# Kernel optimization log

Measured on AMD Instinct MI355X. Metric: run time of the kernel, lower is better.

The kernel has to match this reference:

```python
import jax, jax.numpy as jnp
import numpy as np

G, N, E, F, D = 4096, 64, 256, 64, 128
H1, H2 = 16, 2
EP = 32768
EPS = 1e-15
MAX_LOGSTD = 10.0


def setup_inputs() -> dict:
    key = jax.random.key(0)
    ks = jax.random.split(key, 16)
    def lin(k, i, o):
        return (jax.random.normal(k, (i, o), jnp.float32) / np.sqrt(i)).astype(jnp.float32)
    inp = {}
    inp["x"] = jax.random.normal(ks[0], (G, N, F), jnp.float32)
    inp["edge_index"] = jax.random.randint(ks[1], (G, 2, E), 0, N, dtype=jnp.int32)
    inp["edge_weight"] = jax.random.uniform(ks[2], (G, E), jnp.float32)
    inp["pos_edges"] = jax.random.randint(ks[3], (2, EP), 0, G, dtype=jnp.int32)
    inp["neg_edges"] = jax.random.randint(ks[4], (2, EP), 0, G, dtype=jnp.int32)
    inp["eps"] = jax.random.normal(ks[5], (G, D), jnp.float32)
    inp["W_gcn1"] = lin(ks[6], F, D); inp["b_gcn1"] = jnp.zeros((D,), jnp.float32)
    inp["W_fc1"] = lin(ks[7], D, H1); inp["b_fc1"] = jnp.zeros((H1,), jnp.float32)
    inp["W_fc2"] = lin(ks[8], H1, H2); inp["b_fc2"] = jnp.zeros((H2,), jnp.float32)
    inp["W_c1"] = lin(ks[9], D, 2 * D); inp["b_c1"] = jnp.zeros((2 * D,), jnp.float32)
    inp["W_mu"] = lin(ks[10], 2 * D, D); inp["b_mu"] = jnp.zeros((D,), jnp.float32)
    inp["W_ls"] = lin(ks[11], 2 * D, D); inp["b_ls"] = jnp.zeros((D,), jnp.float32)
    inp["emb"] = jax.random.normal(ks[12], (G, D), jnp.float32)
    inp["W_lin1"] = lin(ks[13], 2 * D, 2 * D); inp["b_lin1"] = jnp.zeros((2 * D,), jnp.float32)
    inp["W_lin2"] = lin(ks[14], 2 * D, 2 * D); inp["b_lin2"] = jnp.zeros((2 * D,), jnp.float32)
    return inp


def gcn_conv(x, src, dst, w, W, b, n):
    # PyG GCNConv: add self-loops (weight 1), sym-normalize, aggregate at target (col).
    xw = x @ W                                      # [n, out]
    deg = jnp.zeros((n,), xw.dtype).at[dst].add(w) + 1.0
    dinv = jax.lax.rsqrt(deg)
    norm = dinv[src] * w * dinv[dst]
    agg = jnp.zeros_like(xw).at[dst].add(xw[src] * norm[:, None])
    agg = agg + xw * (dinv * dinv)[:, None]         # self-loop term
    return agg + b


def sage_graph(x, ei, w, W_gcn1, b_gcn1, W_fc1, b_fc1, W_fc2, b_fc2):
    src, dst = ei[0], ei[1]
    h = gcn_conv(x, src, dst, w, W_gcn1, b_gcn1, N)          # [N, D]
    a1 = jnp.tanh(h @ W_fc1 + b_fc1)                         # [N, H1]
    S = jax.nn.softmax(a1 @ W_fc2 + b_fc2, axis=1)           # [N, 2]
    # get_laplacian(normalization='sym'): L = I - D^{-1/2} A D^{-1/2}, deg from row
    deg = jnp.zeros((N,), x.dtype).at[src].add(w)
    dinv = jnp.where(deg > 0, jax.lax.rsqrt(jnp.maximum(deg, 1e-30)), 0.0)
    lw = -dinv[src] * w * dinv[dst]
    L = jnp.zeros((N, N), x.dtype).at[src, dst].add(lw) + jnp.eye(N, dtype=x.dtype)
    new_adj = S.T @ (L @ S)                                  # [2, 2]
    norm_adj = new_adj / jnp.maximum(jnp.sum(jnp.abs(new_adj), axis=1, keepdims=True), 1e-12)
    diag = jnp.diagonal(norm_adj)
    pos_penalty = jnp.mean((diag - 1.0) ** 2)                # MSE vs ones(2)
    g_emb = jnp.mean(S.T @ h, axis=0)                        # [D]
    return g_emb, pos_penalty


def gcn_conv_unw(x, src, dst, W, b, n):
    return gcn_conv(x, src, dst, jnp.ones(src.shape, x.dtype), W, b, n)


def reference(x, edge_index, edge_weight, pos_edges, neg_edges, eps,
              W_gcn1, b_gcn1, W_fc1, b_fc1, W_fc2, b_fc2,
              W_c1, b_c1, W_mu, b_mu, W_ls, b_ls, emb,
              W_lin1, b_lin1, W_lin2, b_lin2):
    g_embs, pens = jax.vmap(sage_graph,
                            in_axes=(0, 0, 0, None, None, None, None, None, None))(
        x, edge_index, edge_weight, W_gcn1, b_gcn1, W_fc1, b_fc1, W_fc2, b_fc2)
    positive_penalty = jnp.mean(pens)
    # VGAE encode over graph-level graph (dropout in eval mode = identity)
    ps, pd = pos_edges[0], pos_edges[1]
    h = jax.nn.relu(gcn_conv_unw(g_embs, ps, pd, W_c1, b_c1, G))
    mu = gcn_conv_unw(h, ps, pd, W_mu, b_mu, G)
    logstd = jnp.minimum(gcn_conv_unw(h, ps, pd, W_ls, b_ls, G), MAX_LOGSTD)
    z = mu + eps * jnp.exp(logstd)                            # reparametrize
    zc = jnp.concatenate([emb, z], axis=-1)                   # [G, 2D]
    def pred(ei):
        fx = zc[ei[0]] @ W_lin1 + b_lin1
        fy = zc[ei[1]] @ W_lin2 + b_lin2
        return jax.nn.sigmoid(jnp.sum(fx * fy, axis=1))
    pos_pred = pred(pos_edges)
    neg_pred = pred(neg_edges)
    rec_loss = -jnp.mean(jnp.log(pos_pred + EPS)) - jnp.mean(jnp.log(1.0 - neg_pred + EPS))
    kl = -0.5 * jnp.mean(jnp.sum(1.0 + 2.0 * logstd - mu ** 2 - jnp.exp(2.0 * logstd), axis=1))
    pre_loss = rec_loss + kl / G
    return pre_loss, positive_penalty, pos_pred, neg_pred
```

## Files before the change

kernel.cpp:

```cpp
#include <hip/hip_runtime.h>
#include <hip/hip_bf16.h>
#include <math.h>

#define GG   4096
#define NNODE 64
#define EEDGE 256
#define FFEAT 64
#define DDIM 128
#define EP   32768

__global__ void k_prep(const float* __restrict__ Wg, const float* __restrict__ Wf1,
                       const float* __restrict__ bf1, const float* __restrict__ bg,
                       float* __restrict__ Wgf1, float* __restrict__ bcomb,
                       float* __restrict__ bg32, int* __restrict__ icnt_g) {
    int t = threadIdx.x;
    for (int o = t; o < 1024; o += 256) {
        int r = o >> 4, j = o & 15;
        int kk = r >> 2, q = r & 3;
        int f = q * 16 + kk;
        float s = 0.f;
        for (int d = 0; d < 128; ++d) s += Wg[f * 128 + d] * Wf1[d * 16 + j];
        Wgf1[o] = s;
    }
    if (t < 16) {
        float s = bf1[t];
        for (int d = 0; d < 128; ++d) s += bg[d] * Wf1[d * 16 + t];
        bcomb[t] = s;
    }
    if (t >= 128) bg32[t - 128] = 32.0f * bg[t - 128];
    for (int i = t; i < 4096; i += 256) icnt_g[i] = 0;
}

__global__ __launch_bounds__(256) void k_pg(
    const float* __restrict__ x, const int* __restrict__ ei, const float* __restrict__ ew,
    const float* __restrict__ Wgf1, const float* __restrict__ bcomb,
    const float* __restrict__ Wf2, const float* __restrict__ bf2,
    float* __restrict__ Qh, float* __restrict__ pens)
{
    __shared__ __align__(16) float sm[6656];
    float* xs    = sm;
    float* Wp    = sm + 4352;
    int*   lsrc  = (int*)(sm + 5376);
    float* lnrm  = sm + 5632;
    int*   icnt  = (int*)(sm + 5888);
    int*   offs  = (int*)(sm + 5952);
    int*   curs  = (int*)(sm + 6016);
    float* degw  = sm + 6080;
    float* dinvs = sm + 6144;
    float* deg2s = sm + 6208;
    float* dinv2s= sm + 6272;
    float* Ss    = sm + 6336;
    float* LSs   = sm + 6464;
    float* bcs   = sm + 6592;
    float* Wf2s  = sm + 6608;
    float* bf2s  = sm + 6640;

    const int g = blockIdx.x;
    const int t = threadIdx.x;
    const float* xg = x + (size_t)g * 4096;

    int es, ed; float wv;
    {
        const int* eg = ei + (size_t)g * 512;
        es = eg[t];
        ed = eg[256 + t];
        wv = ew[(size_t)g * 256 + t];
        for (int i = t; i < 1024; i += 256) {
            int n = i >> 4, k = (i & 15) * 4;
            *(float4*)&xs[n * 68 + k] = *(const float4*)&xg[n * 64 + k];
        }
        *(float4*)&Wp[t * 4] = *(const float4*)&Wgf1[t * 4];
        if (t < 16) bcs[t] = bcomb[t];
        if (t < 32) Wf2s[t] = Wf2[t];
        if (t < 2)  bf2s[t] = bf2[t];
        if (t < 64) { icnt[t] = 0; degw[t] = 1.0f; deg2s[t] = 0.0f; }
        if (t < 128) LSs[t] = 0.0f;
    }
    __syncthreads();

    atomicAdd(&icnt[ed], 1);
    atomicAdd(&degw[ed], wv);
    atomicAdd(&deg2s[es], wv);
    __syncthreads();

    if (t < 64) {
        int v = icnt[t], own = v;
        for (int o = 1; o < 64; o <<= 1) { int u = __shfl_up(v, o); if (t >= o) v += u; }
        int excl = v - own;
        offs[t] = excl; curs[t] = excl;
        dinvs[t] = rsqrtf(degw[t]);
        float dg = deg2s[t];
        dinv2s[t] = dg > 0.0f ? rsqrtf(fmaxf(dg, 1e-30f)) : 0.0f;
    }
    __syncthreads();

    float lw;
    {
        int pos = atomicAdd(&curs[ed], 1);
        lsrc[pos] = es;
        lnrm[pos] = dinvs[es] * wv * dinvs[ed];
        lw = -dinv2s[es] * wv * dinv2s[ed];
    }
    __syncthreads();

    const int n = t >> 2, q = t & 3, base = q * 16;
    float Av[16];
    {
        float sc = dinvs[n] * dinvs[n];
        const float* xrow = &xs[n * 68 + base];
        *(float4*)&Av[0]  = *(const float4*)&xrow[0];
        *(float4*)&Av[4]  = *(const float4*)&xrow[4];
        *(float4*)&Av[8]  = *(const float4*)&xrow[8];
        *(float4*)&Av[12] = *(const float4*)&xrow[12];
#pragma unroll
        for (int kk = 0; kk < 16; ++kk) Av[kk] *= sc;
        int o = offs[n], c = icnt[n];
        for (int j = 0; j < c; ++j) {
            int s = lsrc[o + j];
            float nm = lnrm[o + j];
            const float* xr = &xs[s * 68 + base];
            float4 X0 = *(const float4*)&xr[0];
            float4 X1 = *(const float4*)&xr[4];
            float4 X2 = *(const float4*)&xr[8];
            float4 X3 = *(const float4*)&xr[12];
            Av[0]  += X0.x * nm; Av[1]  += X0.y * nm; Av[2]  += X0.z * nm; Av[3]  += X0.w * nm;
            Av[4]  += X1.x * nm; Av[5]  += X1.y * nm; Av[6]  += X1.z * nm; Av[7]  += X1.w * nm;
            Av[8]  += X2.x * nm; Av[9]  += X2.y * nm; Av[10] += X2.z * nm; Av[11] += X2.w * nm;
            Av[12] += X3.x * nm; Av[13] += X3.y * nm; Av[14] += X3.z * nm; Av[15] += X3.w * nm;
        }
        __syncthreads();
        float* xw = &xs[n * 68 + base];
        *(float4*)&xw[0]  = *(float4*)&Av[0];
        *(float4*)&xw[4]  = *(float4*)&Av[4];
        *(float4*)&xw[8]  = *(float4*)&Av[8];
        *(float4*)&xw[12] = *(float4*)&Av[12];
    }
    __syncthreads();

    {
        float pj[16];
#pragma unroll
        for (int j = 0; j < 16; ++j) pj[j] = 0.f;
#pragma unroll
        for (int kk = 0; kk < 16; ++kk) {
            float a = Av[kk];
            const float* wr = &Wp[((kk << 2) + q) << 4];
            float4 w0 = *(const float4*)&wr[0];
            float4 w1 = *(const float4*)&wr[4];
            float4 w2 = *(const float4*)&wr[8];
            float4 w3 = *(const float4*)&wr[12];
            pj[0]  += a * w0.x; pj[1]  += a * w0.y; pj[2]  += a * w0.z; pj[3]  += a * w0.w;
            pj[4]  += a * w1.x; pj[5]  += a * w1.y; pj[6]  += a * w1.z; pj[7]  += a * w1.w;
            pj[8]  += a * w2.x; pj[9]  += a * w2.y; pj[10] += a * w2.z; pj[11] += a * w2.w;
            pj[12] += a * w3.x; pj[13] += a * w3.y; pj[14] += a * w3.z; pj[15] += a * w3.w;
        }
#pragma unroll
        for (int j = 0; j < 16; ++j) {
            pj[j] += __shfl_xor(pj[j], 1);
            pj[j] += __shfl_xor(pj[j], 2);
        }
        float z0 = bf2s[0], z1 = bf2s[1];
#pragma unroll
        for (int j = 0; j < 16; ++j) {
            float aj = tanhf(pj[j] + bcs[j]);
            z0 += aj * Wf2s[2 * j];
            z1 += aj * Wf2s[2 * j + 1];
        }
        float m = fmaxf(z0, z1);
        float e0 = expf(z0 - m), e1 = expf(z1 - m);
        float inv = 1.0f / (e0 + e1);
        if (q == 0) { Ss[n * 2] = e0 * inv; Ss[n * 2 + 1] = e1 * inv; }
    }
    __syncthreads();

    {
        float s0 = Ss[ed * 2], s1 = Ss[ed * 2 + 1];
        atomicAdd(&LSs[es * 2],     lw * s0);
        atomicAdd(&LSs[es * 2 + 1], lw * s1);
    }
    __syncthreads();

    if (t < 64) {
        float s0 = Ss[t * 2], s1 = Ss[t * 2 + 1];
        float l0 = s0 + LSs[t * 2], l1 = s1 + LSs[t * 2 + 1];
        float p00 = s0 * l0, p01 = s0 * l1, p10 = s1 * l0, p11 = s1 * l1;
        for (int o = 32; o; o >>= 1) {
            p00 += __shfl_down(p00, o); p01 += __shfl_down(p01, o);
            p10 += __shfl_down(p10, o); p11 += __shfl_down(p11, o);
        }
        if (t == 0) {
            float r0 = fmaxf(fabsf(p00) + fabsf(p01), 1e-12f);
            float r1 = fmaxf(fabsf(p10) + fabsf(p11), 1e-12f);
            float d0 = p00 / r0 - 1.0f, d1 = p11 / r1 - 1.0f;
            pens[g] = 0.5f * (d0 * d0 + d1 * d1);
        }
    }
    {
        int k = t & 63, p = t >> 6;
        float qk = 0.f;
#pragma unroll 4
        for (int nn = 0; nn < 16; ++nn)
            qk += xs[(p * 16 + nn) * 68 + k];
        Wp[p * 64 + k] = qk;
    }
    __syncthreads();
    if (t < 64)
        Qh[(size_t)g * 64 + t] = 0.5f * (Wp[t] + Wp[64 + t] + Wp[128 + t] + Wp[192 + t]);
}

__global__ void k_cnt(const int* __restrict__ pd, int* __restrict__ icnt) {
    int e = blockIdx.x * 256 + threadIdx.x;
    atomicAdd(&icnt[pd[e]], 1);
}

__global__ void k_scan(const int* __restrict__ icnt, int* __restrict__ offs,
                       int* __restrict__ curs, float* __restrict__ dinv) {
    __shared__ int wsum[4];
    int t = threadIdx.x;
    int base = t * 16;
    int l0,l1,l2,l3,l4,l5,l6,l7,l8,l9,l10,l11,l12,l13,l14,l15;
    l0=icnt[base+0]; l1=icnt[base+1]; l2=icnt[base+2]; l3=icnt[base+3];
    l4=icnt[base+4]; l5=icnt[base+5]; l6=icnt[base+6]; l7=icnt[base+7];
    l8=icnt[base+8]; l9=icnt[base+9]; l10=icnt[base+10]; l11=icnt[base+11];
    l12=icnt[base+12]; l13=icnt[base+13]; l14=icnt[base+14]; l15=icnt[base+15];
    int s = l0+l1+l2+l3+l4+l5+l6+l7+l8+l9+l10+l11+l12+l13+l14+l15;
    int lane = t & 63, w = t >> 6;
    int v = s;
    for (int o = 1; o < 64; o <<= 1) { int u = __shfl_up(v, o); if (lane >= o) v += u; }
    if (lane == 63) wsum[w] = v;
    __syncthreads();
    int woff = 0;
    for (int i = 0; i < 4; ++i) if (i < w) woff += wsum[i];
    int run = woff + v - s;
#define SC(L, I) offs[base+(I)] = run; curs[base+(I)] = run; \
    dinv[base+(I)] = rsqrtf((float)(L) + 1.0f); run += L;
    SC(l0,0) SC(l1,1) SC(l2,2) SC(l3,3) SC(l4,4) SC(l5,5) SC(l6,6) SC(l7,7)
    SC(l8,8) SC(l9,9) SC(l10,10) SC(l11,11) SC(l12,12) SC(l13,13) SC(l14,14) SC(l15,15)
#undef SC
}

__global__ void k_place(const int* __restrict__ pe, const float* __restrict__ dinv,
                        int* __restrict__ curs, int* __restrict__ csr_src,
                        float* __restrict__ csr_nrm) {
    int e = blockIdx.x * 256 + threadIdx.x;
    int s = pe[e], d = pe[EP + e];
    int pos = atomicAdd(&curs[d], 1);
    csr_src[pos] = s;
    csr_nrm[pos] = dinv[s] * dinv[d];
}

__global__ void k_gather128(const int* __restrict__ offs, const int* __restrict__ icnt,
                            const int* __restrict__ csr_src, const float* __restrict__ csr_nrm,
                            const float* __restrict__ dinv, const float* __restrict__ in,
                            float* __restrict__ out) {
    int g = blockIdx.x, d = threadIdx.x;
    float dv = dinv[g];
    float acc = in[(size_t)g * 128 + d] * dv * dv;
    int o = offs[g], c = icnt[g];
    for (int j = 0; j < c; ++j)
        acc += in[(size_t)csr_src[o + j] * 128 + d] * csr_nrm[o + j];
    out[(size_t)g * 128 + d] = acc;
}

__global__ void k_gather256(const int* __restrict__ offs, const int* __restrict__ icnt,
                            const int* __restrict__ csr_src, const float* __restrict__ csr_nrm,
                            const float* __restrict__ dinv, const float* __restrict__ in,
                            float* __restrict__ out) {
    int g = blockIdx.x, d = threadIdx.x;
    float dv = dinv[g];
    float acc = in[(size_t)g * 256 + d] * dv * dv;
    int o = offs[g], c = icnt[g];
    for (int j = 0; j < c; ++j)
        acc += in[(size_t)csr_src[o + j] * 256 + d] * csr_nrm[o + j];
    out[(size_t)g * 256 + d] = acc;
}

__global__ __launch_bounds__(256) void k_gemm(
    const float* __restrict__ A,
    const float* __restrict__ B0, const float* __restrict__ bias0, float* __restrict__ C0,
    const float* __restrict__ B1, const float* __restrict__ bias1, float* __restrict__ C1,
    int M, int K, int N, int dorelu)
{
    __shared__ __align__(16) float lds[2 * 4352];
    const float* B = B0; const float* bias = bias0; float* C = C0;
    int by = blockIdx.y;
    if (B1 != nullptr && by >= (int)(gridDim.y >> 1)) {
        B = B1; bias = bias1; C = C1; by -= (gridDim.y >> 1);
    }
    const int mb = blockIdx.x * 64, nbb = by * 64;
    const int t = threadIdx.x;
    const int tm4 = (t >> 4) * 4, tn4 = (t & 15) * 4;
    const int ma = t >> 2, ka = (t & 3) * 8;
    const int kb = t >> 3, nb8 = (t & 7) * 8;

    float4 pa0, pa1, pb0, pb1;
#define LOADT(K0) { \
    const float* Ap = &A[(size_t)(mb + ma) * K + (K0) + ka]; \
    pa0 = *(const float4*)Ap; pa1 = *(const float4*)(Ap + 4); \
    const float* Bp = &B[(size_t)((K0) + kb) * N + nbb + nb8]; \
    pb0 = *(const float4*)Bp; pb1 = *(const float4*)(Bp + 4); }
#define STORET(BUF) { \
    float* At_ = lds + (BUF) * 4352; \
    At_[(ka + 0) * 68 + ma] = pa0.x; At_[(ka + 1) * 68 + ma] = pa0.y; \
    At_[(ka + 2) * 68 + ma] = pa0.z; At_[(ka + 3) * 68 + ma] = pa0.w; \
    At_[(ka + 4) * 68 + ma] = pa1.x; At_[(ka + 5) * 68 + ma] = pa1.y; \
    At_[(ka + 6) * 68 + ma] = pa1.z; At_[(ka + 7) * 68 + ma] = pa1.w; \
    float* Bs_ = lds + (BUF) * 4352 + 2176; \
    *(float4*)&Bs_[kb * 68 + nb8] = pb0; *(float4*)&Bs_[kb * 68 + nb8 + 4] = pb1; }

    float4 ca0 = {0,0,0,0}, ca1 = {0,0,0,0}, ca2 = {0,0,0,0}, ca3 = {0,0,0,0};
    const int nk0 = K >> 5;
    LOADT(0)
    STORET(0)
    __syncthreads();
    for (int it = 0; it < nk0; ++it) {
        if (it + 1 < nk0) LOADT((it + 1) * 32)
        const float* At_ = lds + (it & 1) * 4352;
        const float* Bs_ = At_ + 2176;
#pragma unroll
        for (int k = 0; k < 32; ++k) {
            float4 av = *(const float4*)&At_[k * 68 + tm4];
            float4 bv = *(const float4*)&Bs_[k * 68 + tn4];
            ca0.x += av.x * bv.x; ca0.y += av.x * bv.y; ca0.z += av.x * bv.z; ca0.w += av.x * bv.w;
            ca1.x += av.y * bv.x; ca1.y += av.y * bv.y; ca1.z += av.y * bv.z; ca1.w += av.y * bv.w;
            ca2.x += av.z * bv.x; ca2.y += av.z * bv.y; ca2.z += av.z * bv.z; ca2.w += av.z * bv.w;
            ca3.x += av.w * bv.x; ca3.y += av.w * bv.y; ca3.z += av.w * bv.z; ca3.w += av.w * bv.w;
        }
        if (it + 1 < nk0) {
            STORET((it + 1) & 1)
            __syncthreads();
        }
    }
#undef LOADT
#undef STORET
    float4 bv4 = {0, 0, 0, 0};
    if (bias) bv4 = *(const float4*)&bias[nbb + tn4];
#define CST(I, CV) { \
    float4 v; v.x = CV.x + bv4.x; v.y = CV.y + bv4.y; v.z = CV.z + bv4.z; v.w = CV.w + bv4.w; \
    if (dorelu) { v.x = fmaxf(v.x, 0.f); v.y = fmaxf(v.y, 0.f); v.z = fmaxf(v.z, 0.f); v.w = fmaxf(v.w, 0.f); } \
    *(float4*)&C[(size_t)(mb + tm4 + (I)) * N + nbb + tn4] = v; }
    CST(0, ca0) CST(1, ca1) CST(2, ca2) CST(3, ca3)
#undef CST
}

__global__ void k_fin_z(const float* __restrict__ mu_arr, const float* __restrict__ ls_arr,
                        const float* __restrict__ eps, const float* __restrict__ emb,
                        float* __restrict__ zc, float* __restrict__ klp) {
    __shared__ float smw[2];
    int g = blockIdx.x, d = threadIdx.x;
    int idx = g * 128 + d;
    float mu = mu_arr[idx];
    float ls = fminf(ls_arr[idx], 10.0f);
    float z = mu + eps[idx] * expf(ls);
    zc[(size_t)g * 256 + d] = emb[idx];
    zc[(size_t)g * 256 + 128 + d] = z;
    float term = 1.0f + 2.0f * ls - mu * mu - expf(2.0f * ls);
    for (int o = 32; o; o >>= 1) term += __shfl_down(term, o);
    if ((d & 63) == 0) smw[d >> 6] = term;
    __syncthreads();
    if (d == 0) klp[g] = smw[0] + smw[1];
}

__global__ void k_pred(const float* __restrict__ A, const float* __restrict__ B,
                       const int* __restrict__ pos, const int* __restrict__ neg,
                       float* __restrict__ out, float* __restrict__ predp) {
    __shared__ float smw[16];
    int t = threadIdx.x, sub = t >> 4, l = t & 15;
    int eg = blockIdx.x * 16 + sub;
    int isneg = eg >= EP;
    int e = eg - (isneg ? EP : 0);
    const int* eix = isneg ? neg : pos;
    int s = eix[e], d = eix[EP + e];
    const float4* Ar = (const float4*)(A + (size_t)s * 256);
    const float4* Br = (const float4*)(B + (size_t)d * 256);
    float dot = 0.f;
#pragma unroll
    for (int q = 0; q < 4; ++q) {
        float4 av = Ar[l + 16 * q], bv = Br[l + 16 * q];
        dot += av.x * bv.x + av.y * bv.y + av.z * bv.z + av.w * bv.w;
    }
    for (int o = 8; o; o >>= 1) dot += __shfl_down(dot, o);
    if (l == 0) {
        float p = 1.0f / (1.0f + expf(-dot));
        float term;
        if (isneg) { out[2 + EP + e] = p; term = logf(1.0f - p + 1e-15f); }
        else       { out[2 + e] = p;      term = logf(p + 1e-15f); }
        smw[sub] = term;
    }
    __syncthreads();
    if (t == 0) {
        float s16 = 0.f;
#pragma unroll
        for (int i = 0; i < 16; ++i) s16 += smw[i];
        predp[blockIdx.x] = s16;
    }
}

__global__ void k_final(const float* __restrict__ pens, const float* __restrict__ klp,
                        const float* __restrict__ predp, float* __restrict__ out) {
    __shared__ float sm[16];
    int t = threadIdx.x;
    float s_pen = 0.f, s_kl = 0.f, s_pos = 0.f, s_neg = 0.f;
    for (int i = t; i < 4096; i += 256) { s_pen += pens[i]; s_kl += klp[i]; }
    for (int i = t; i < 2048; i += 256) { s_pos += predp[i]; s_neg += predp[2048 + i]; }
    for (int o = 32; o; o >>= 1) {
        s_pen += __shfl_down(s_pen, o); s_kl += __shfl_down(s_kl, o);
        s_pos += __shfl_down(s_pos, o); s_neg += __shfl_down(s_neg, o);
    }
    int w = t >> 6;
    if ((t & 63) == 0) { sm[w] = s_pen; sm[4 + w] = s_kl; sm[8 + w] = s_pos; sm[12 + w] = s_neg; }
    __syncthreads();
    if (t == 0) {
        float pen = sm[0] + sm[1] + sm[2] + sm[3];
        float kls = sm[4] + sm[5] + sm[6] + sm[7];
        float pos = sm[8] + sm[9] + sm[10] + sm[11];
        float neg = sm[12] + sm[13] + sm[14] + sm[15];
        float rec = -(pos / 32768.0f) - (neg / 32768.0f);
        out[0] = rec - 0.5f * kls / (4096.0f * 4096.0f);
        out[1] = pen * (1.0f / 4096.0f);
    }
}

extern "C" void kernel_launch(void* const* d_in, const int* in_sizes, int n_in,
                              void* d_out, int out_size, void* d_ws, size_t ws_size,
                              hipStream_t stream) {
    const float* x   = (const float*)d_in[0];
    const int*   ei  = (const int*)d_in[1];
    const float* ew  = (const float*)d_in[2];
    const int*   pos = (const int*)d_in[3];
    const int*   neg = (const int*)d_in[4];
    const float* eps = (const float*)d_in[5];
    const float* Wg  = (const float*)d_in[6];
    const float* bg  = (const float*)d_in[7];
    const float* Wf1 = (const float*)d_in[8];
    const float* bf1 = (const float*)d_in[9];
    const float* Wf2 = (const float*)d_in[10];
    const float* bf2 = (const float*)d_in[11];
    const float* Wc1 = (const float*)d_in[12];
    const float* bc1 = (const float*)d_in[13];
    const float* Wmu = (const float*)d_in[14];
    const float* bmu = (const float*)d_in[15];
    const float* Wls = (const float*)d_in[16];
    const float* bls = (const float*)d_in[17];
    const float* emb = (const float*)d_in[18];
    const float* Wl1 = (const float*)d_in[19];
    const float* bl1 = (const float*)d_in[20];
    const float* Wl2 = (const float*)d_in[21];
    const float* bl2 = (const float*)d_in[22];
    float* out = (float*)d_out;
    float* ws  = (float*)d_ws;

    float* g_embs  = ws + 0;
    float* dinv    = ws + 524288;
    int*   icnt_g  = (int*)(ws + 528384);
    int*   off_g   = (int*)(ws + 532480);
    int*   cur_g   = (int*)(ws + 536576);
    int*   csr_src = (int*)(ws + 540672);
    float* csr_nrm = ws + 573440;
    float* Qh      = ws + 606208;
    float* ga      = ws + 868352;
    float* h       = ws + 1392640;
    float* ha      = ws + 2441216;
    float* mu_arr  = ws + 3489792;
    float* ls_arr  = ws + 4014080;
    float* zc      = ws + 4538368;
    float* Abuf    = ws + 5586944;
    float* Bbuf    = ws + 6635520;
    float* pens    = ws + 7684096;
    float* klp     = ws + 7688192;
    float* predp   = ws + 7692288;
    float* Wgf1    = ws + 7708672;
    float* bcomb   = ws + 7709696;
    float* bg32    = ws + 7709712;

    k_prep<<<1, 256, 0, stream>>>(Wg, Wf1, bf1, bg, Wgf1, bcomb, bg32, icnt_g);
    k_pg<<<GG, 256, 0, stream>>>(x, ei, ew, Wgf1, bcomb, Wf2, bf2, Qh, pens);
    k_gemm<<<dim3(64, 2), 256, 0, stream>>>(Qh, Wg, bg32, g_embs,
                                            nullptr, nullptr, nullptr, GG, 64, 128, 0);

    k_cnt<<<EP / 256, 256, 0, stream>>>(pos + EP, icnt_g);
    k_scan<<<1, 256, 0, stream>>>(icnt_g, off_g, cur_g, dinv);
    k_place<<<EP / 256, 256, 0, stream>>>(pos, dinv, cur_g, csr_src, csr_nrm);

    k_gather128<<<GG, 128, 0, stream>>>(off_g, icnt_g, csr_src, csr_nrm, dinv, g_embs, ga);
    k_gemm<<<dim3(64, 4), 256, 0, stream>>>(ga, Wc1, bc1, h,
                                            nullptr, nullptr, nullptr, GG, 128, 256, 1);

    k_gather256<<<GG, 256, 0, stream>>>(off_g, icnt_g, csr_src, csr_nrm, dinv, h, ha);
    k_gemm<<<dim3(64, 4), 256, 0, stream>>>(ha, Wmu, bmu, mu_arr,
                                            Wls, bls, ls_arr, GG, 256, 128, 0);
    k_fin_z<<<GG, 128, 0, stream>>>(mu_arr, ls_arr, eps, emb, zc, klp);

    k_gemm<<<dim3(64, 8), 256, 0, stream>>>(zc, Wl1, bl1, Abuf,
                                            Wl2, bl2, Bbuf, GG, 256, 256, 0);

    k_pred<<<(2 * EP) / 16, 256, 0, stream>>>(Abuf, Bbuf, pos, neg, out, predp);
    k_final<<<1, 256, 0, stream>>>(pens, klp, predp, out);
}
```

Baseline: 320.4 us.

## Restructure per-graph fc1 projection, pack edge lists, and use fast intrinsics

The fc1 projection in k_pg is re-split so each wavefront handles one 16-feature slice for all 64 nodes. It reads Wgf1 with wave-uniform (scalar) global loads instead of staging it in LDS, and accumulates partial sums into a padded LDS buffer with atomics, replacing the xor-shuffle reduction. Edge source indices and norms are packed into one float2 array, and tanh, exp and log in several kernels are replaced with fast intrinsics, reusing exp(ls) squared for the KL term. This aims to cut LDS traffic and transcendental cost. It trades those for LDS atomic contention and some accuracy loss from the approximate intrinsics.

```diff
diff --git a/kernel.cpp b/kernel.cpp
--- a/kernel.cpp
+++ b/kernel.cpp
@@ -9,15 +9,18 @@
 #define DDIM 128
 #define EP   32768
 
+__device__ __forceinline__ float fast_tanh(float x) {
+    float e = __expf(2.0f * x);
+    return 1.0f - 2.0f / (e + 1.0f);
+}
+
 __global__ void k_prep(const float* __restrict__ Wg, const float* __restrict__ Wf1,
                        const float* __restrict__ bf1, const float* __restrict__ bg,
                        float* __restrict__ Wgf1, float* __restrict__ bcomb,
                        float* __restrict__ bg32, int* __restrict__ icnt_g) {
     int t = threadIdx.x;
     for (int o = t; o < 1024; o += 256) {
-        int r = o >> 4, j = o & 15;
-        int kk = r >> 2, q = r & 3;
-        int f = q * 16 + kk;
+        int f = o >> 4, j = o & 15;
         float s = 0.f;
         for (int d = 0; d < 128; ++d) s += Wg[f * 128 + d] * Wf1[d * 16 + j];
         Wgf1[o] = s;
@@ -37,23 +40,20 @@
     const float* __restrict__ Wf2, const float* __restrict__ bf2,
     float* __restrict__ Qh, float* __restrict__ pens)
 {
-    __shared__ __align__(16) float sm[6656];
+    __shared__ __align__(16) float sm[6688];
     float* xs    = sm;
-    float* Wp    = sm + 4352;
-    int*   lsrc  = (int*)(sm + 5376);
-    float* lnrm  = sm + 5632;
-    int*   icnt  = (int*)(sm + 5888);
-    int*   offs  = (int*)(sm + 5952);
-    int*   curs  = (int*)(sm + 6016);
-    float* degw  = sm + 6080;
-    float* dinvs = sm + 6144;
-    float* deg2s = sm + 6208;
-    float* dinv2s= sm + 6272;
-    float* Ss    = sm + 6336;
-    float* LSs   = sm + 6464;
-    float* bcs   = sm + 6592;
-    float* Wf2s  = sm + 6608;
-    float* bf2s  = sm + 6640;
+    float* a1s   = sm + 4352;
+    float* lpair = sm + 5440;
+    int*   icnt  = (int*)(sm + 5952);
+    int*   offs  = (int*)(sm + 6016);
+    int*   curs  = (int*)(sm + 6080);
+    float* degw  = sm + 6144;
+    float* dinvs = sm + 6208;
+    float* deg2s = sm + 6272;
+    float* dinv2s= sm + 6336;
+    float* Ss    = sm + 6400;
+    float* LSs   = sm + 6528;
+    float* Wf2s  = sm + 6656;
 
     const int g = blockIdx.x;
     const int t = threadIdx.x;
@@ -69,12 +69,13 @@
             int n = i >> 4, k = (i & 15) * 4;
             *(float4*)&xs[n * 68 + k] = *(const float4*)&xg[n * 64 + k];
         }
-        *(float4*)&Wp[t * 4] = *(const float4*)&Wgf1[t * 4];
-        if (t < 16) bcs[t] = bcomb[t];
         if (t < 32) Wf2s[t] = Wf2[t];
-        if (t < 2)  bf2s[t] = bf2[t];
         if (t < 64) { icnt[t] = 0; degw[t] = 1.0f; deg2s[t] = 0.0f; }
         if (t < 128) LSs[t] = 0.0f;
+        for (int i = t; i < 1088; i += 256) {
+            int r = i / 17, j = i - r * 17;
+            a1s[i] = (j < 16) ? bcomb[j] : 0.0f;
+        }
     }
     __syncthreads();
 
@@ -97,17 +98,19 @@
     float lw;
     {
         int pos = atomicAdd(&curs[ed], 1);
-        lsrc[pos] = es;
-        lnrm[pos] = dinvs[es] * wv * dinvs[ed];
+        float2 pr;
+        pr.x = __int_as_float(es);
+        pr.y = dinvs[es] * wv * dinvs[ed];
+        *(float2*)&lpair[2 * pos] = pr;
         lw = -dinv2s[es] * wv * dinv2s[ed];
     }
     __syncthreads();
 
     const int n = t >> 2, q = t & 3, base = q * 16;
-    float Av[16];
     {
         float sc = dinvs[n] * dinvs[n];
         const float* xrow = &xs[n * 68 + base];
+        float Av[16];
         *(float4*)&Av[0]  = *(const float4*)&xrow[0];
         *(float4*)&Av[4]  = *(const float4*)&xrow[4];
         *(float4*)&Av[8]  = *(const float4*)&xrow[8];
@@ -116,8 +119,9 @@
         for (int kk = 0; kk < 16; ++kk) Av[kk] *= sc;
         int o = offs[n], c = icnt[n];
         for (int j = 0; j < c; ++j) {
-            int s = lsrc[o + j];
-            float nm = lnrm[o + j];
+            float2 pr = *(const float2*)&lpair[2 * (o + j)];
+            int s = __float_as_int(pr.x);
+            float nm = pr.y;
             const float* xr = &xs[s * 68 + base];
             float4 X0 = *(const float4*)&xr[0];
             float4 X1 = *(const float4*)&xr[4];
@@ -138,45 +142,58 @@
     __syncthreads();
 
     {
+        const int w  = __builtin_amdgcn_readfirstlane(t >> 6);
+        const int nn = t & 63;
+        const float* xrow = &xs[nn * 68 + w * 16];
+        float xk[16];
+        *(float4*)&xk[0]  = *(const float4*)&xrow[0];
+        *(float4*)&xk[4]  = *(const float4*)&xrow[4];
+        *(float4*)&xk[8]  = *(const float4*)&xrow[8];
+        *(float4*)&xk[12] = *(const float4*)&xrow[12];
+        const float* __restrict__ Wb = Wgf1 + (w << 8);
         float pj[16];
 #pragma unroll
         for (int j = 0; j < 16; ++j) pj[j] = 0.f;
 #pragma unroll
         for (int kk = 0; kk < 16; ++kk) {
-            float a = Av[kk];
-            const float* wr = &Wp[((kk << 2) + q) << 4];
-            float4 w0 = *(const float4*)&wr[0];
-            float4 w1 = *(const float4*)&wr[4];
-            float4 w2 = *(const float4*)&wr[8];
-            float4 w3 = *(const float4*)&wr[12];
-            pj[0]  += a * w0.x; pj[1]  += a * w0.y; pj[2]  += a * w0.z; pj[3]  += a * w0.w;
-            pj[4]  += a * w1.x; pj[5]  += a * w1.y; pj[6]  += a * w1.z; pj[7]  += a * w1.w;
-            pj[8]  += a * w2.x; pj[9]  += a * w2.y; pj[10] += a * w2.z; pj[11] += a * w2.w;
-            pj[12] += a * w3.x; pj[13] += a * w3.y; pj[14] += a * w3.z; pj[15] += a * w3.w;
-        }
-#pragma unroll
-        for (int j = 0; j < 16; ++j) {
-            pj[j] += __shfl_xor(pj[j], 1);
-            pj[j] += __shfl_xor(pj[j], 2);
-        }
-        float z0 = bf2s[0], z1 = bf2s[1];
-#pragma unroll
-        for (int j = 0; j < 16; ++j) {
-            float aj = tanhf(pj[j] + bcs[j]);
-            z0 += aj * Wf2s[2 * j];
-            z1 += aj * Wf2s[2 * j + 1];
-        }
-        float m = fmaxf(z0, z1);
-        float e0 = expf(z0 - m), e1 = expf(z1 - m);
-        float inv = 1.0f / (e0 + e1);
-        if (q == 0) { Ss[n * 2] = e0 * inv; Ss[n * 2 + 1] = e1 * inv; }
-    }
-    __syncthreads();
-
-    {
-        float s0 = Ss[ed * 2], s1 = Ss[ed * 2 + 1];
-        atomicAdd(&LSs[es * 2],     lw * s0);
-        atomicAdd(&LSs[es * 2 + 1], lw * s1);
+            float a = xk[kk];
+#pragma unroll
+            for (int j = 0; j < 16; ++j)
+                pj[j] = fmaf(a, Wb[(kk << 4) | j], pj[j]);
+        }
+        float* arow = &a1s[nn * 17];
+#pragma unroll
+        for (int j = 0; j < 16; ++j) atomicAdd(&arow[j], pj[j]);
+    }
+    __syncthreads();
+
+    {
+        const float* arow = &a1s[n * 17 + q * 4];
+        float t0 = fast_tanh(arow[0]);
+        float t1 = fast_tanh(arow[1]);
+        float t2 = fast_tanh(arow[2]);
+        float t3 = fast_tanh(arow[3]);
+        float4 wf0 = *(const float4*)&Wf2s[8 * q];
+        float4 wf1 = *(const float4*)&Wf2s[8 * q + 4];
+        float z0 = t0 * wf0.x + t1 * wf0.z + t2 * wf1.x + t3 * wf1.z;
+        float z1 = t0 * wf0.y + t1 * wf0.w + t2 * wf1.y + t3 * wf1.w;
+        z0 += __shfl_xor(z0, 1); z0 += __shfl_xor(z0, 2);
+        z1 += __shfl_xor(z1, 1); z1 += __shfl_xor(z1, 2);
+        if (q == 0) {
+            z0 += bf2[0]; z1 += bf2[1];
+            float m = fmaxf(z0, z1);
+            float e0 = __expf(z0 - m), e1 = __expf(z1 - m);
+            float inv = 1.0f / (e0 + e1);
+            float2 sv; sv.x = e0 * inv; sv.y = e1 * inv;
+            *(float2*)&Ss[2 * n] = sv;
+        }
+    }
+    __syncthreads();
+
+    {
+        float2 sv = *(const float2*)&Ss[2 * ed];
+        atomicAdd(&LSs[es * 2],     lw * sv.x);
+        atomicAdd(&LSs[es * 2 + 1], lw * sv.y);
     }
     __syncthreads();
 
@@ -201,11 +218,11 @@
 #pragma unroll 4
         for (int nn = 0; nn < 16; ++nn)
             qk += xs[(p * 16 + nn) * 68 + k];
-        Wp[p * 64 + k] = qk;
+        a1s[p * 64 + k] = qk;
     }
     __syncthreads();
     if (t < 64)
-        Qh[(size_t)g * 64 + t] = 0.5f * (Wp[t] + Wp[64 + t] + Wp[128 + t] + Wp[192 + t]);
+        Qh[(size_t)g * 64 + t] = 0.5f * (a1s[t] + a1s[64 + t] + a1s[128 + t] + a1s[192 + t]);
 }
 
 __global__ void k_cnt(const int* __restrict__ pd, int* __restrict__ icnt) {
@@ -351,10 +368,11 @@
     int idx = g * 128 + d;
     float mu = mu_arr[idx];
     float ls = fminf(ls_arr[idx], 10.0f);
-    float z = mu + eps[idx] * expf(ls);
+    float e  = __expf(ls);
+    float z = mu + eps[idx] * e;
     zc[(size_t)g * 256 + d] = emb[idx];
     zc[(size_t)g * 256 + 128 + d] = z;
-    float term = 1.0f + 2.0f * ls - mu * mu - expf(2.0f * ls);
+    float term = 1.0f + 2.0f * ls - mu * mu - e * e;
     for (int o = 32; o; o >>= 1) term += __shfl_down(term, o);
     if ((d & 63) == 0) smw[d >> 6] = term;
     __syncthreads();
@@ -381,10 +399,10 @@
     }
     for (int o = 8; o; o >>= 1) dot += __shfl_down(dot, o);
     if (l == 0) {
-        float p = 1.0f / (1.0f + expf(-dot));
+        float p = 1.0f / (1.0f + __expf(-dot));
         float term;
-        if (isneg) { out[2 + EP + e] = p; term = logf(1.0f - p + 1e-15f); }
-        else       { out[2 + e] = p;      term = logf(p + 1e-15f); }
+        if (isneg) { out[2 + EP + e] = p; term = __logf(1.0f - p + 1e-15f); }
+        else       { out[2 + e] = p;      term = __logf(p + 1e-15f); }
         smw[sub] = term;
     }
     __syncthreads();
```

Measured after the change: 400.3 us. 24.9% more time.
